# Performance work log

Measured on AMD Instinct MI355X. Metric: run time of the kernel, lower is better.

Reference implementation:

```python
import jax, jax.numpy as jnp
import numpy as np

N_NODES = 50000
N_EDGES = 800000
IN_FEATS = 128
HIDDEN = 128
OUT_LEN = 128


def setup_inputs() -> dict:
    key = jax.random.key(0)
    ks = jax.random.split(key, 8)
    feat = jax.random.normal(ks[0], (N_NODES, IN_FEATS), dtype=jnp.float32)
    # Glorot-ish init for weights, zeros for bias (DGL GraphConv default)
    def w(k, fi, fo):
        return jax.random.normal(k, (fi, fo), dtype=jnp.float32) / np.sqrt(fi)
    W1 = w(ks[1], IN_FEATS, HIDDEN)
    W2 = w(ks[2], HIDDEN, HIDDEN)
    W3 = w(ks[3], HIDDEN, OUT_LEN)
    b1 = jnp.zeros((HIDDEN,), jnp.float32)
    b2 = jnp.zeros((HIDDEN,), jnp.float32)
    b3 = jnp.zeros((OUT_LEN,), jnp.float32)
    src = jax.random.randint(ks[4], (N_EDGES,), 0, N_NODES, dtype=jnp.int32)
    dst = jax.random.randint(ks[5], (N_EDGES,), 0, N_NODES, dtype=jnp.int32)
    return {"feat": feat, "W1": W1, "b1": b1, "W2": W2, "b2": b2,
            "W3": W3, "b3": b3, "src": src, "dst": dst}


def _degree_norm(idx, n):
    # degree counts, clamped to min 1 (DGL behavior), then ^{-1/2}
    deg = jax.ops.segment_sum(jnp.ones_like(idx, dtype=jnp.float32), idx,
                              num_segments=n)
    return jax.lax.rsqrt(jnp.maximum(deg, 1.0))


def _graph_conv(x, W, b, src, dst, out_norm, in_norm):
    # DGL GraphConv, norm='both':
    # h = D_dst^{-1/2} * segsum_dst( D_src^{-1/2} * x[src] ) @ W + b
    h = x * out_norm[:, None]
    m = jax.ops.segment_sum(h[src], dst, num_segments=x.shape[0])  # [N, d]
    m = m * in_norm[:, None]
    return m @ W + b


def reference(feat, W1, b1, W2, b2, W3, b3, src, dst):
    out_norm = _degree_norm(src, feat.shape[0])  # out-degree norm (source)
    in_norm = _degree_norm(dst, feat.shape[0])   # in-degree norm (dest)
    h = jax.nn.relu(_graph_conv(feat, W1, b1, src, dst, out_norm, in_norm))
    h = jax.nn.relu(_graph_conv(h, W2, b2, src, dst, out_norm, in_norm))
    h = _graph_conv(h, W3, b3, src, dst, out_norm, in_norm)
    # single graph: mean_nodes == mean over all nodes, then squeeze -> [out_len]
    return jnp.mean(h, axis=0)
```

## Files before the change

kernel.cpp:

```cpp
#include <hip/hip_runtime.h>

#define N_NODES 50000
#define N_EDGES 800000
#define F 128
#define SCAN_NB 49
#define RN_NB 196
#define CH 64
#define EPC (N_EDGES / CH)
#define HALF 25000
#define QTR 12500
#define BSTRIDE 17
#define AGG_NB (N_NODES / 4)
#define GB ((N_NODES + 63) / 64)

typedef __bf16 bf16x8 __attribute__((ext_vector_type(8)));
typedef float  f32x4  __attribute__((ext_vector_type(4)));
typedef float  f32x2  __attribute__((ext_vector_type(2)));

__device__ inline unsigned short f2bf(float f) {
    unsigned u = __float_as_uint(f);
    u += 0x7FFF + ((u >> 16) & 1);
    return (unsigned short)(u >> 16);
}
__device__ inline unsigned packbf2(float a, float b) {
    return (unsigned)f2bf(a) | ((unsigned)f2bf(b) << 16);
}

__device__ inline void fp8x8_to_f32(uint2 u, float* f) {
    f32x2 v0 = __builtin_amdgcn_cvt_pk_f32_fp8(u.x, false);
    f32x2 v1 = __builtin_amdgcn_cvt_pk_f32_fp8(u.x, true);
    f32x2 v2 = __builtin_amdgcn_cvt_pk_f32_fp8(u.y, false);
    f32x2 v3 = __builtin_amdgcn_cvt_pk_f32_fp8(u.y, true);
    f[0] = v0.x; f[1] = v0.y; f[2] = v1.x; f[3] = v1.y;
    f[4] = v2.x; f[5] = v2.y; f[6] = v3.x; f[7] = v3.y;
}
__device__ inline unsigned f32x4_to_fp8(float a, float b, float c, float d) {
    unsigned r = __builtin_amdgcn_cvt_pk_fp8_f32(a, b, 0, false);
    r = __builtin_amdgcn_cvt_pk_fp8_f32(c, d, r, true);
    return r;
}

__global__ __launch_bounds__(1024) void hist_kernel(const int* __restrict__ src,
                                                    const int* __restrict__ dst,
                                                    unsigned short* __restrict__ Hs16,
                                                    unsigned short* __restrict__ Hd16) {
    __shared__ unsigned hist[HALF / 2];
    int bx = blockIdx.x;
    int c = bx >> 2, t = bx & 1, h = (bx >> 1) & 1;
    const int* ids = t ? dst : src;
    unsigned short* H = t ? Hd16 : Hs16;
    int base = h * HALF;
    for (int j = threadIdx.x; j < HALF / 2; j += 1024) hist[j] = 0;
    __syncthreads();
    int e0 = c * EPC;
    for (int e = e0 + threadIdx.x; e < e0 + EPC; e += 1024) {
        int id = ids[e] - base;
        if ((unsigned)id < (unsigned)HALF)
            atomicAdd(&hist[id >> 1], 1u << ((id & 1) * 16));
    }
    __syncthreads();
    for (int j = threadIdx.x; j < HALF / 2; j += 1024)
        *(unsigned*)&H[(size_t)c * N_NODES + base + 2 * j] = hist[j];
}

__global__ __launch_bounds__(256) void reduceN_kernel(const unsigned short* __restrict__ Hs16,
                                                      const unsigned short* __restrict__ Hd16,
                                                      float* __restrict__ onorm,
                                                      float* __restrict__ inorm,
                                                      int* __restrict__ degd,
                                                      int* __restrict__ bsums) {
    __shared__ int wsum[4];
    int i = blockIdx.x * 256 + threadIdx.x;
    int dd = 0;
    if (i < N_NODES) {
        int ds = 0;
        for (int c = 0; c < CH; c++) {
            ds += Hs16[(size_t)c * N_NODES + i];
            dd += Hd16[(size_t)c * N_NODES + i];
        }
        onorm[i] = rsqrtf(fmaxf((float)ds, 1.0f));
        inorm[i] = rsqrtf(fmaxf((float)dd, 1.0f));
        degd[i] = dd;
    }
    int v = dd;
#pragma unroll
    for (int off = 32; off; off >>= 1) v += __shfl_down(v, off);
    if ((threadIdx.x & 63) == 0) wsum[threadIdx.x >> 6] = v;
    __syncthreads();
    if (threadIdx.x == 0)
        bsums[blockIdx.x] = wsum[0] + wsum[1] + wsum[2] + wsum[3];
}

__global__ __launch_bounds__(1024) void tq_kernel(const int* __restrict__ src,
                                                  const int* __restrict__ dst,
                                                  const float* __restrict__ inorm,
                                                  float* __restrict__ Tq,
                                                  const float* __restrict__ feat,
                                                  const float* __restrict__ onorm,
                                                  uint2* __restrict__ xq,
                                                  const float* __restrict__ W1,
                                                  const float* __restrict__ W2,
                                                  unsigned short* __restrict__ Wt) {
    __shared__ float a[QTR];
    int bx = blockIdx.x;
    int c = bx >> 2, q = bx & 3;
    int base = q * QTR;
    for (int j = threadIdx.x; j < QTR; j += 1024) a[j] = 0.0f;
    __syncthreads();
    int e0 = c * EPC;
    for (int e = e0 + threadIdx.x; e < e0 + EPC; e += 1024) {
        int s = src[e] - base;
        if ((unsigned)s < (unsigned)QTR)
            atomicAdd(&a[s], inorm[dst[e]]);
    }
    __syncthreads();
    for (int j = threadIdx.x; j < QTR; j += 1024)
        Tq[(size_t)c * N_NODES + base + j] = a[j];

    int T = gridDim.x * 1024;
    int id0 = bx * 1024 + threadIdx.x;
    for (int i = id0; i < N_NODES * F / 8; i += T) {
        float w = onorm[i >> 4];
        const float4* xv = (const float4*)feat;
        float4 v0 = xv[i * 2], v1 = xv[i * 2 + 1];
        uint2 o;
        o.x = f32x4_to_fp8(v0.x * w, v0.y * w, v0.z * w, v0.w * w);
        o.y = f32x4_to_fp8(v1.x * w, v1.y * w, v1.z * w, v1.w * w);
        xq[i] = o;
    }
    for (int i = id0; i < 2 * F * F; i += T) {
        int wi = i >> 14, rem = i & 16383;
        int n = rem >> 7, k = rem & 127;
        const float* W = wi ? W2 : W1;
        Wt[(size_t)wi * F * F + (size_t)n * F + k] = f2bf(W[k * F + n]);
    }
}

__global__ __launch_bounds__(1024) void scanC_kernel(const int* __restrict__ deg,
                                                     const int* __restrict__ bsums,
                                                     int* __restrict__ rowst,
                                                     const unsigned short* __restrict__ Hd16,
                                                     int* __restrict__ P,
                                                     const float* __restrict__ Tq,
                                                     float* __restrict__ qt) {
    __shared__ int wsum[16];
    int t = threadIdx.x, lane = t & 63, w = t >> 6;
    int i = blockIdx.x * 1024 + t;
    int v = (i < N_NODES) ? deg[i] : 0;
    int incl = v;
#pragma unroll
    for (int off = 1; off < 64; off <<= 1) {
        int u = __shfl_up(incl, off);
        if (lane >= off) incl += u;
    }
    if (lane == 63) wsum[w] = incl;
    __syncthreads();
    if (t == 0) {
        int s = 0;
        int kmax = min(4 * (int)blockIdx.x, RN_NB);
        for (int k = 0; k < kmax; k++) s += bsums[k];
#pragma unroll
        for (int k = 0; k < 16; k++) { int x = wsum[k]; wsum[k] = s; s += x; }
    }
    __syncthreads();
    incl += wsum[w];
    if (i < N_NODES) {
        int s = incl - v;
        rowst[i] = s;
        if (i == N_NODES - 1) rowst[N_NODES] = incl;
        float tsum = 0.0f;
        for (int c = 0; c < CH; c++) {
            size_t o = (size_t)c * N_NODES + i;
            P[o] = s; s += Hd16[o];
            tsum += Tq[o];
        }
        qt[i] = tsum;
    }
}

__global__ __launch_bounds__(1024) void scatter2_kernel(const int* __restrict__ src,
                                                        const int* __restrict__ dst,
                                                        const int* __restrict__ P,
                                                        int* __restrict__ esrc) {
    __shared__ int cur[QTR];
    int bx = blockIdx.x;
    int c = bx >> 2, q = bx & 3;
    int base = q * QTR;
    for (int j = threadIdx.x; j < QTR; j += 1024)
        cur[j] = P[(size_t)c * N_NODES + base + j];
    __syncthreads();
    int e0 = c * EPC;
    for (int e = e0 + threadIdx.x; e < e0 + EPC; e += 1024) {
        int d = dst[e] - base;
        if ((unsigned)d < (unsigned)QTR) {
            int pos = atomicAdd(&cur[d], 1);
            esrc[pos] = src[e];
        }
    }
}

__global__ __launch_bounds__(256) void agg_csr_kernel(const uint2* __restrict__ xq,
                                                      uint4* __restrict__ mb,
                                                      const int* __restrict__ rowst,
                                                      const int* __restrict__ esrc,
                                                      const float* __restrict__ inorm) {
    int w = threadIdx.x >> 6;
    int lane = threadIdx.x & 63;
    int g = lane >> 4, t = lane & 15;
    int row = blockIdx.x * 4 + w;
    int beg = __builtin_amdgcn_readfirstlane(rowst[row]);
    int end = __builtin_amdgcn_readfirstlane(rowst[row + 1]);
    float acc[8];
#pragma unroll
    for (int k = 0; k < 8; k++) acc[k] = 0.0f;

    for (int e = beg; e < end; e += 16) {
        int ea = min(e + g,      end - 1);
        int eb = min(e + 4 + g,  end - 1);
        int ec = min(e + 8 + g,  end - 1);
        int ed = min(e + 12 + g, end - 1);
        int sa = esrc[ea], sb = esrc[eb], sc = esrc[ec], sd = esrc[ed];
        uint2 ua = xq[(size_t)sa * 16 + t];
        uint2 ub = xq[(size_t)sb * 16 + t];
        uint2 uc = xq[(size_t)sc * 16 + t];
        uint2 ud = xq[(size_t)sd * 16 + t];
        float wa = (e + g      < end) ? 1.0f : 0.0f;
        float wb = (e + 4 + g  < end) ? 1.0f : 0.0f;
        float wc = (e + 8 + g  < end) ? 1.0f : 0.0f;
        float wd = (e + 12 + g < end) ? 1.0f : 0.0f;
        float fa[8], fb[8], fc[8], fd[8];
        fp8x8_to_f32(ua, fa); fp8x8_to_f32(ub, fb);
        fp8x8_to_f32(uc, fc); fp8x8_to_f32(ud, fd);
#pragma unroll
        for (int k = 0; k < 8; k++)
            acc[k] += fa[k] * wa + fb[k] * wb + fc[k] * wc + fd[k] * wd;
    }
#pragma unroll
    for (int k = 0; k < 8; k++) {
        acc[k] += __shfl_xor(acc[k], 16, 64);
        acc[k] += __shfl_xor(acc[k], 32, 64);
    }
    if (g == 0) {
        float inw = inorm[row];
        uint4 o;
        o.x = packbf2(acc[0] * inw, acc[1] * inw);
        o.y = packbf2(acc[2] * inw, acc[3] * inw);
        o.z = packbf2(acc[4] * inw, acc[5] * inw);
        o.w = packbf2(acc[6] * inw, acc[7] * inw);
        mb[(size_t)row * 16 + t] = o;
    }
}

template <int FINAL>
__global__ __launch_bounds__(256) void mfma_gemm_kernel(const unsigned short* __restrict__ A,
                                                        const unsigned short* __restrict__ Wt,
                                                        const float* __restrict__ bias,
                                                        const float* __restrict__ onorm,
                                                        unsigned char* __restrict__ Y8,
                                                        const float* __restrict__ qt,
                                                        float* __restrict__ part2) {
    __shared__ uint4 sB[F * BSTRIDE];
    __shared__ float sPf[4][F];
    int tid = threadIdx.x;
    int w = tid >> 6;
    int lane = tid & 63;
    int quad = lane >> 4, r16 = lane & 15;
    int row0 = blockIdx.x * 64 + w * 16;

    const uint4* Arow = (const uint4*)(A + (size_t)(row0 + r16) * F);
    uint4 a[4];
#pragma unroll
    for (int kk = 0; kk < 4; kk++) a[kk] = Arow[kk * 4 + quad];

    const uint4* G = (const uint4*)Wt;
    for (int j = tid; j < F * 16; j += 256)
        sB[(j >> 4) * BSTRIDE + (j & 15)] = G[j];

    f32x4 acc[8];
#pragma unroll
    for (int t = 0; t < 8; t++) acc[t] = (f32x4){0.f, 0.f, 0.f, 0.f};
    __syncthreads();

#pragma unroll
    for (int kk = 0; kk < 4; kk++) {
        bf16x8 av = __builtin_bit_cast(bf16x8, a[kk]);
#pragma unroll
        for (int t = 0; t < 8; t++) {
            bf16x8 bv = __builtin_bit_cast(bf16x8,
                sB[(t * 16 + r16) * BSTRIDE + kk * 4 + quad]);
            acc[t] = __builtin_amdgcn_mfma_f32_16x16x32_bf16(av, bv, acc[t], 0, 0, 0);
        }
    }

    float rw[4];
#pragma unroll
    for (int reg = 0; reg < 4; reg++) {
        int row = row0 + quad * 4 + reg;
        rw[reg] = (row < N_NODES) ? (FINAL ? qt[row] * onorm[row] : onorm[row]) : 0.0f;
    }

    if (!FINAL) {
#pragma unroll
        for (int t = 0; t < 8; t++) {
            int col = t * 16 + r16;
            float bb = bias[col];
#pragma unroll
            for (int reg = 0; reg < 4; reg++) {
                int row = row0 + quad * 4 + reg;
                if (row < N_NODES) {
                    float v = fmaxf(acc[t][reg] + bb, 0.0f) * rw[reg];
                    unsigned p = __builtin_amdgcn_cvt_pk_fp8_f32(v, v, 0, false);
                    Y8[(size_t)row * F + col] = (unsigned char)(p & 0xFF);
                }
            }
        }
    } else {
#pragma unroll
        for (int t = 0; t < 8; t++) {
            int col = t * 16 + r16;
            float bb = bias[col];
            float p = 0.0f;
#pragma unroll
            for (int reg = 0; reg < 4; reg++)
                p += fmaxf(acc[t][reg] + bb, 0.0f) * rw[reg];
            p += __shfl_xor(p, 16, 64);
            p += __shfl_xor(p, 32, 64);
            if (quad == 0) sPf[w][col] = p;
        }
        __syncthreads();
        if (tid < F)
            part2[(size_t)blockIdx.x * F + tid] =
                sPf[0][tid] + sPf[1][tid] + sPf[2][tid] + sPf[3][tid];
    }
}

__global__ __launch_bounds__(1024) void final_kernel(const float* __restrict__ part2,
                                                     const float* __restrict__ W3,
                                                     const float* __restrict__ b3,
                                                     float* __restrict__ out) {
    __shared__ float sc[8][F];
    int tid = threadIdx.x;
    int col = tid & 127, sl = tid >> 7;
    float acc = 0.0f;
    for (int b = sl; b < GB; b += 8) acc += part2[(size_t)b * F + col];
    sc[sl][col] = acc;
    __syncthreads();
    if (tid < F) {
        float s = 0.0f;
#pragma unroll
        for (int k = 0; k < 8; k++) s += sc[k][tid];
        sc[0][tid] = s * (1.0f / (float)N_NODES);
    }
    __syncthreads();
    if (tid < F) {
        float o = b3[tid];
        for (int k = 0; k < F; k++) o += sc[0][k] * W3[k * F + tid];
        out[tid] = o;
    }
}

extern "C" void kernel_launch(void* const* d_in, const int* in_sizes, int n_in,
                              void* d_out, int out_size, void* d_ws, size_t ws_size,
                              hipStream_t stream) {
    const float* feat = (const float*)d_in[0];
    const float* W1   = (const float*)d_in[1];
    const float* b1   = (const float*)d_in[2];
    const float* W2   = (const float*)d_in[3];
    const float* b2   = (const float*)d_in[4];
    const float* W3   = (const float*)d_in[5];
    const float* b3   = (const float*)d_in[6];
    const int*   src  = (const int*)d_in[7];
    const int*   dst  = (const int*)d_in[8];
    float* out = (float*)d_out;

    char* ws = (char*)d_ws;
    size_t off = 0;
    uint4* mb    = (uint4*)(ws + off); off += (size_t)N_NODES * F * 2;
    float* Tq    = (float*)(ws + off); off += (size_t)CH * N_NODES * 4;
    int*   P     = (int*)  (ws + off); off += (size_t)CH * N_NODES * 4;
    unsigned short* Hs16 = (unsigned short*)(ws + off); off += (size_t)CH * N_NODES * 2;
    unsigned short* Hd16 = (unsigned short*)(ws + off); off += (size_t)CH * N_NODES * 2;
    uint2* xq    = (uint2*)(ws + off); off += (size_t)N_NODES * F;
    uint2* hq    = (uint2*)(ws + off); off += (size_t)N_NODES * F;
    unsigned short* Wt = (unsigned short*)(ws + off); off += 2 * F * F * 2;
    float* part2 = (float*)(ws + off); off += (size_t)GB * F * 4;
    int*   esrc  = (int*)  (ws + off); off += (size_t)N_EDGES * 4;
    float* onorm = (float*)(ws + off); off += N_NODES * 4;
    float* inorm = (float*)(ws + off); off += N_NODES * 4;
    float* qt    = (float*)(ws + off); off += N_NODES * 4;
    int*   degd  = (int*)  (ws + off); off += N_NODES * 4;
    int*   rowst = (int*)  (ws + off); off += (N_NODES + 1) * 4;
    int*   bsums = (int*)  (ws + off); off += 256 * 4;

    hist_kernel<<<4 * CH, 1024, 0, stream>>>(src, dst, Hs16, Hd16);
    reduceN_kernel<<<RN_NB, 256, 0, stream>>>(Hs16, Hd16, onorm, inorm, degd, bsums);
    tq_kernel<<<4 * CH, 1024, 0, stream>>>(src, dst, inorm, Tq,
                                           feat, onorm, xq, W1, W2, Wt);
    scanC_kernel<<<SCAN_NB, 1024, 0, stream>>>(degd, bsums, rowst, Hd16, P, Tq, qt);
    scatter2_kernel<<<4 * CH, 1024, 0, stream>>>(src, dst, P, esrc);

    agg_csr_kernel<<<AGG_NB, 256, 0, stream>>>(xq, mb, rowst, esrc, inorm);
    mfma_gemm_kernel<0><<<GB, 256, 0, stream>>>((const unsigned short*)mb, Wt, b1,
                                                onorm, (unsigned char*)hq, qt, part2);
    agg_csr_kernel<<<AGG_NB, 256, 0, stream>>>(hq, mb, rowst, esrc, inorm);
    mfma_gemm_kernel<1><<<GB, 256, 0, stream>>>((const unsigned short*)mb, Wt + F * F,
                                                b2, onorm, (unsigned char*)hq, qt, part2);
    final_kernel<<<1, 1024, 0, stream>>>(part2, W3, b3, out);
}
```

Before: 233.0 us.

## Fuse qt accumulation into CSR scatter with global atomics, drop tq kernel

Removes the separate tq pass that built per-chunk partial sums of inorm[dst] per source node in shared memory. Those sums are now accumulated with global float atomics inside the scatter kernel, which also absorbs the fp8 feature quantization and weight transpose. This saves one kernel launch, one pass over the edges and the 64x-node Tq buffer, at the cost of 800k global atomics with contention. It also clamps the GEMM's A-row index so out-of-range rows in the last block no longer read past the buffer.

```diff
diff --git a/kernel.cpp b/kernel.cpp
--- a/kernel.cpp
+++ b/kernel.cpp
@@ -91,31 +91,75 @@
         bsums[blockIdx.x] = wsum[0] + wsum[1] + wsum[2] + wsum[3];
 }
 
-__global__ __launch_bounds__(1024) void tq_kernel(const int* __restrict__ src,
-                                                  const int* __restrict__ dst,
-                                                  const float* __restrict__ inorm,
-                                                  float* __restrict__ Tq,
-                                                  const float* __restrict__ feat,
-                                                  const float* __restrict__ onorm,
-                                                  uint2* __restrict__ xq,
-                                                  const float* __restrict__ W1,
-                                                  const float* __restrict__ W2,
-                                                  unsigned short* __restrict__ Wt) {
-    __shared__ float a[QTR];
+__global__ __launch_bounds__(1024) void scanC_kernel(const int* __restrict__ deg,
+                                                     const int* __restrict__ bsums,
+                                                     int* __restrict__ rowst,
+                                                     const unsigned short* __restrict__ Hd16,
+                                                     int* __restrict__ P,
+                                                     float* __restrict__ qtacc) {
+    __shared__ int wsum[16];
+    int t = threadIdx.x, lane = t & 63, w = t >> 6;
+    int i = blockIdx.x * 1024 + t;
+    int v = (i < N_NODES) ? deg[i] : 0;
+    int incl = v;
+#pragma unroll
+    for (int off = 1; off < 64; off <<= 1) {
+        int u = __shfl_up(incl, off);
+        if (lane >= off) incl += u;
+    }
+    if (lane == 63) wsum[w] = incl;
+    __syncthreads();
+    if (t == 0) {
+        int s = 0;
+        int kmax = min(4 * (int)blockIdx.x, RN_NB);
+        for (int k = 0; k < kmax; k++) s += bsums[k];
+#pragma unroll
+        for (int k = 0; k < 16; k++) { int x = wsum[k]; wsum[k] = s; s += x; }
+    }
+    __syncthreads();
+    incl += wsum[w];
+    if (i < N_NODES) {
+        int s = incl - v;
+        rowst[i] = s;
+        if (i == N_NODES - 1) rowst[N_NODES] = incl;
+        qtacc[i] = 0.0f;
+        for (int c = 0; c < CH; c++) {
+            size_t o = (size_t)c * N_NODES + i;
+            P[o] = s; s += Hd16[o];
+        }
+    }
+}
+
+__global__ __launch_bounds__(1024) void scatter2_kernel(const int* __restrict__ src,
+                                                        const int* __restrict__ dst,
+                                                        const int* __restrict__ P,
+                                                        int* __restrict__ esrc,
+                                                        const float* __restrict__ inorm,
+                                                        float* __restrict__ qtacc,
+                                                        const float* __restrict__ feat,
+                                                        const float* __restrict__ onorm,
+                                                        uint2* __restrict__ xq,
+                                                        const float* __restrict__ W1,
+                                                        const float* __restrict__ W2,
+                                                        unsigned short* __restrict__ Wt) {
+    __shared__ int cur[QTR];
     int bx = blockIdx.x;
     int c = bx >> 2, q = bx & 3;
     int base = q * QTR;
-    for (int j = threadIdx.x; j < QTR; j += 1024) a[j] = 0.0f;
+    for (int j = threadIdx.x; j < QTR; j += 1024)
+        cur[j] = P[(size_t)c * N_NODES + base + j];
     __syncthreads();
     int e0 = c * EPC;
     for (int e = e0 + threadIdx.x; e < e0 + EPC; e += 1024) {
-        int s = src[e] - base;
-        if ((unsigned)s < (unsigned)QTR)
-            atomicAdd(&a[s], inorm[dst[e]]);
-    }
-    __syncthreads();
-    for (int j = threadIdx.x; j < QTR; j += 1024)
-        Tq[(size_t)c * N_NODES + base + j] = a[j];
+        int dv = dst[e];
+        int d = dv - base;
+        if ((unsigned)d < (unsigned)QTR) {
+            int s = src[e];
+            int pos = atomicAdd(&cur[d], 1);
+            esrc[pos] = s;
+            atomicAdd(&qtacc[s], inorm[dv]);
+        }
+    }
 
     int T = gridDim.x * 1024;
     int id0 = bx * 1024 + threadIdx.x;
@@ -133,69 +177,6 @@
         int n = rem >> 7, k = rem & 127;
         const float* W = wi ? W2 : W1;
         Wt[(size_t)wi * F * F + (size_t)n * F + k] = f2bf(W[k * F + n]);
-    }
-}
-
-__global__ __launch_bounds__(1024) void scanC_kernel(const int* __restrict__ deg,
-                                                     const int* __restrict__ bsums,
-                                                     int* __restrict__ rowst,
-                                                     const unsigned short* __restrict__ Hd16,
-                                                     int* __restrict__ P,
-                                                     const float* __restrict__ Tq,
-                                                     float* __restrict__ qt) {
-    __shared__ int wsum[16];
-    int t = threadIdx.x, lane = t & 63, w = t >> 6;
-    int i = blockIdx.x * 1024 + t;
-    int v = (i < N_NODES) ? deg[i] : 0;
-    int incl = v;
-#pragma unroll
-    for (int off = 1; off < 64; off <<= 1) {
-        int u = __shfl_up(incl, off);
-        if (lane >= off) incl += u;
-    }
-    if (lane == 63) wsum[w] = incl;
-    __syncthreads();
-    if (t == 0) {
-        int s = 0;
-        int kmax = min(4 * (int)blockIdx.x, RN_NB);
-        for (int k = 0; k < kmax; k++) s += bsums[k];
-#pragma unroll
-        for (int k = 0; k < 16; k++) { int x = wsum[k]; wsum[k] = s; s += x; }
-    }
-    __syncthreads();
-    incl += wsum[w];
-    if (i < N_NODES) {
-        int s = incl - v;
-        rowst[i] = s;
-        if (i == N_NODES - 1) rowst[N_NODES] = incl;
-        float tsum = 0.0f;
-        for (int c = 0; c < CH; c++) {
-            size_t o = (size_t)c * N_NODES + i;
-            P[o] = s; s += Hd16[o];
-            tsum += Tq[o];
-        }
-        qt[i] = tsum;
-    }
-}
-
-__global__ __launch_bounds__(1024) void scatter2_kernel(const int* __restrict__ src,
-                                                        const int* __restrict__ dst,
-                                                        const int* __restrict__ P,
-                                                        int* __restrict__ esrc) {
-    __shared__ int cur[QTR];
-    int bx = blockIdx.x;
-    int c = bx >> 2, q = bx & 3;
-    int base = q * QTR;
-    for (int j = threadIdx.x; j < QTR; j += 1024)
-        cur[j] = P[(size_t)c * N_NODES + base + j];
-    __syncthreads();
-    int e0 = c * EPC;
-    for (int e = e0 + threadIdx.x; e < e0 + EPC; e += 1024) {
-        int d = dst[e] - base;
-        if ((unsigned)d < (unsigned)QTR) {
-            int pos = atomicAdd(&cur[d], 1);
-            esrc[pos] = src[e];
-        }
     }
 }
 
@@ -267,7 +248,8 @@
     int quad = lane >> 4, r16 = lane & 15;
     int row0 = blockIdx.x * 64 + w * 16;
 
-    const uint4* Arow = (const uint4*)(A + (size_t)(row0 + r16) * F);
+    int arow = min(row0 + r16, N_NODES - 1);
+    const uint4* Arow = (const uint4*)(A + (size_t)arow * F);
     uint4 a[4];
 #pragma unroll
     for (int kk = 0; kk < 4; kk++) a[kk] = Arow[kk * 4 + quad];
@@ -376,7 +358,6 @@
     char* ws = (char*)d_ws;
     size_t off = 0;
     uint4* mb    = (uint4*)(ws + off); off += (size_t)N_NODES * F * 2;
-    float* Tq    = (float*)(ws + off); off += (size_t)CH * N_NODES * 4;
     int*   P     = (int*)  (ws + off); off += (size_t)CH * N_NODES * 4;
     unsigned short* Hs16 = (unsigned short*)(ws + off); off += (size_t)CH * N_NODES * 2;
     unsigned short* Hd16 = (unsigned short*)(ws + off); off += (size_t)CH * N_NODES * 2;
@@ -387,23 +368,22 @@
     int*   esrc  = (int*)  (ws + off); off += (size_t)N_EDGES * 4;
     float* onorm = (float*)(ws + off); off += N_NODES * 4;
     float* inorm = (float*)(ws + off); off += N_NODES * 4;
-    float* qt    = (float*)(ws + off); off += N_NODES * 4;
+    float* qtacc = (float*)(ws + off); off += N_NODES * 4;
     int*   degd  = (int*)  (ws + off); off += N_NODES * 4;
     int*   rowst = (int*)  (ws + off); off += (N_NODES + 1) * 4;
     int*   bsums = (int*)  (ws + off); off += 256 * 4;
 
     hist_kernel<<<4 * CH, 1024, 0, stream>>>(src, dst, Hs16, Hd16);
     reduceN_kernel<<<RN_NB, 256, 0, stream>>>(Hs16, Hd16, onorm, inorm, degd, bsums);
-    tq_kernel<<<4 * CH, 1024, 0, stream>>>(src, dst, inorm, Tq,
-                                           feat, onorm, xq, W1, W2, Wt);
-    scanC_kernel<<<SCAN_NB, 1024, 0, stream>>>(degd, bsums, rowst, Hd16, P, Tq, qt);
-    scatter2_kernel<<<4 * CH, 1024, 0, stream>>>(src, dst, P, esrc);
+    scanC_kernel<<<SCAN_NB, 1024, 0, stream>>>(degd, bsums, rowst, Hd16, P, qtacc);
+    scatter2_kernel<<<4 * CH, 1024, 0, stream>>>(src, dst, P, esrc, inorm, qtacc,
+                                                 feat, onorm, xq, W1, W2, Wt);
 
     agg_csr_kernel<<<AGG_NB, 256, 0, stream>>>(xq, mb, rowst, esrc, inorm);
     mfma_gemm_kernel<0><<<GB, 256, 0, stream>>>((const unsigned short*)mb, Wt, b1,
-                                                onorm, (unsigned char*)hq, qt, part2);
+                                                onorm, (unsigned char*)hq, qtacc, part2);
     agg_csr_kernel<<<AGG_NB, 256, 0, stream>>>(hq, mb, rowst, esrc, inorm);
     mfma_gemm_kernel<1><<<GB, 256, 0, stream>>>((const unsigned short*)mb, Wt + F * F,
-                                                b2, onorm, (unsigned char*)hq, qt, part2);
+                                                b2, onorm, (unsigned char*)hq, qtacc, part2);
     final_kernel<<<1, 1024, 0, stream>>>(part2, W3, b3, out);
 }
```

After: 251.2 us. 7.8% more time.

## Shrink degree histograms to bytes and fuse degree reduction into scan

Applied to the files above, without the earlier changes.

The per-chunk degree histograms are stored as 8-bit counts instead of 16-bit, with four nodes packed per shared-memory atomic word. The per-block degree sums are now produced inside the histogram kernel. This lets the separate reduce kernel be merged into the scan kernel, which now also writes byte-sized per-chunk prefix offsets instead of a full int offset array. The qt reduction moves into the first aggregation kernel, and GEMM row loads are clamped to stay in bounds. The aim is to cut histogram and offset memory traffic and one kernel launch. The cost is that per-chunk counts and per-node in-degrees must fit in 8 bits, which holds only for graphs without heavy-degree nodes.

```diff
diff --git a/kernel.cpp b/kernel.cpp
--- a/kernel.cpp
+++ b/kernel.cpp
@@ -4,7 +4,6 @@
 #define N_EDGES 800000
 #define F 128
 #define SCAN_NB 49
-#define RN_NB 196
 #define CH 64
 #define EPC (N_EDGES / CH)
 #define HALF 25000
@@ -42,53 +41,90 @@
 
 __global__ __launch_bounds__(1024) void hist_kernel(const int* __restrict__ src,
                                                     const int* __restrict__ dst,
-                                                    unsigned short* __restrict__ Hs16,
-                                                    unsigned short* __restrict__ Hd16) {
-    __shared__ unsigned hist[HALF / 2];
+                                                    unsigned char* __restrict__ Hs8,
+                                                    unsigned char* __restrict__ Hd8,
+                                                    int* __restrict__ bsump) {
+    __shared__ unsigned hist[HALF / 4];
     int bx = blockIdx.x;
     int c = bx >> 2, t = bx & 1, h = (bx >> 1) & 1;
     const int* ids = t ? dst : src;
-    unsigned short* H = t ? Hd16 : Hs16;
+    unsigned char* H = t ? Hd8 : Hs8;
     int base = h * HALF;
-    for (int j = threadIdx.x; j < HALF / 2; j += 1024) hist[j] = 0;
+    for (int j = threadIdx.x; j < HALF / 4; j += 1024) hist[j] = 0;
     __syncthreads();
     int e0 = c * EPC;
     for (int e = e0 + threadIdx.x; e < e0 + EPC; e += 1024) {
         int id = ids[e] - base;
         if ((unsigned)id < (unsigned)HALF)
-            atomicAdd(&hist[id >> 1], 1u << ((id & 1) * 16));
-    }
-    __syncthreads();
-    for (int j = threadIdx.x; j < HALF / 2; j += 1024)
-        *(unsigned*)&H[(size_t)c * N_NODES + base + 2 * j] = hist[j];
-}
-
-__global__ __launch_bounds__(256) void reduceN_kernel(const unsigned short* __restrict__ Hs16,
-                                                      const unsigned short* __restrict__ Hd16,
-                                                      float* __restrict__ onorm,
-                                                      float* __restrict__ inorm,
-                                                      int* __restrict__ degd,
-                                                      int* __restrict__ bsums) {
-    __shared__ int wsum[4];
-    int i = blockIdx.x * 256 + threadIdx.x;
+            atomicAdd(&hist[id >> 2], 1u << ((id & 3) * 8));
+    }
+    __syncthreads();
+    unsigned* Hw = (unsigned*)(H + (size_t)c * N_NODES + base);
+    for (int j = threadIdx.x; j < HALF / 4; j += 1024) Hw[j] = hist[j];
+    if (t) {
+        int w = threadIdx.x >> 6, lane = threadIdx.x & 63;
+        for (int r = w; r < SCAN_NB; r += 16) {
+            int gi0 = max(r * 1024, base);
+            int gi1 = min(r * 1024 + 1024, base + HALF);
+            int s = 0;
+            for (int li = gi0 - base + lane; li < gi1 - base; li += 64)
+                s += (hist[li >> 2] >> ((li & 3) * 8)) & 255;
+#pragma unroll
+            for (int off = 32; off; off >>= 1) s += __shfl_down(s, off);
+            if (lane == 0) bsump[(c * 2 + h) * SCAN_NB + r] = s;
+        }
+    }
+}
+
+__global__ __launch_bounds__(1024) void scanC_kernel(const unsigned char* __restrict__ Hs8,
+                                                     const unsigned char* __restrict__ Hd8,
+                                                     const int* __restrict__ bsump,
+                                                     float* __restrict__ onorm,
+                                                     float* __restrict__ inorm,
+                                                     int* __restrict__ rowst,
+                                                     unsigned char* __restrict__ P8) {
+    __shared__ int wsum[16];
+    __shared__ int tot[SCAN_NB];
+    int t = threadIdx.x, lane = t & 63, w = t >> 6;
+    int i = blockIdx.x * 1024 + t;
+    if (t < SCAN_NB) {
+        int s = 0;
+        for (int p = 0; p < 2 * CH; p++) s += bsump[p * SCAN_NB + t];
+        tot[t] = s;
+    }
     int dd = 0;
     if (i < N_NODES) {
-        int ds = 0;
+        int ds = 0, run = 0;
         for (int c = 0; c < CH; c++) {
-            ds += Hs16[(size_t)c * N_NODES + i];
-            dd += Hd16[(size_t)c * N_NODES + i];
-        }
+            size_t o = (size_t)c * N_NODES + i;
+            ds += Hs8[o];
+            P8[o] = (unsigned char)run;
+            run += Hd8[o];
+        }
+        dd = run;
         onorm[i] = rsqrtf(fmaxf((float)ds, 1.0f));
         inorm[i] = rsqrtf(fmaxf((float)dd, 1.0f));
-        degd[i] = dd;
-    }
-    int v = dd;
-#pragma unroll
-    for (int off = 32; off; off >>= 1) v += __shfl_down(v, off);
-    if ((threadIdx.x & 63) == 0) wsum[threadIdx.x >> 6] = v;
-    __syncthreads();
-    if (threadIdx.x == 0)
-        bsums[blockIdx.x] = wsum[0] + wsum[1] + wsum[2] + wsum[3];
+    }
+    int v = dd, incl = v;
+#pragma unroll
+    for (int off = 1; off < 64; off <<= 1) {
+        int u = __shfl_up(incl, off);
+        if (lane >= off) incl += u;
+    }
+    if (lane == 63) wsum[w] = incl;
+    __syncthreads();
+    if (t == 0) {
+        int s = 0;
+        for (int r = 0; r < (int)blockIdx.x; r++) s += tot[r];
+#pragma unroll
+        for (int k = 0; k < 16; k++) { int x = wsum[k]; wsum[k] = s; s += x; }
+    }
+    __syncthreads();
+    incl += wsum[w];
+    if (i < N_NODES) {
+        rowst[i] = incl - v;
+        if (i == N_NODES - 1) rowst[N_NODES] = incl;
+    }
 }
 
 __global__ __launch_bounds__(1024) void tq_kernel(const int* __restrict__ src,
@@ -136,58 +172,17 @@
     }
 }
 
-__global__ __launch_bounds__(1024) void scanC_kernel(const int* __restrict__ deg,
-                                                     const int* __restrict__ bsums,
-                                                     int* __restrict__ rowst,
-                                                     const unsigned short* __restrict__ Hd16,
-                                                     int* __restrict__ P,
-                                                     const float* __restrict__ Tq,
-                                                     float* __restrict__ qt) {
-    __shared__ int wsum[16];
-    int t = threadIdx.x, lane = t & 63, w = t >> 6;
-    int i = blockIdx.x * 1024 + t;
-    int v = (i < N_NODES) ? deg[i] : 0;
-    int incl = v;
-#pragma unroll
-    for (int off = 1; off < 64; off <<= 1) {
-        int u = __shfl_up(incl, off);
-        if (lane >= off) incl += u;
-    }
-    if (lane == 63) wsum[w] = incl;
-    __syncthreads();
-    if (t == 0) {
-        int s = 0;
-        int kmax = min(4 * (int)blockIdx.x, RN_NB);
-        for (int k = 0; k < kmax; k++) s += bsums[k];
-#pragma unroll
-        for (int k = 0; k < 16; k++) { int x = wsum[k]; wsum[k] = s; s += x; }
-    }
-    __syncthreads();
-    incl += wsum[w];
-    if (i < N_NODES) {
-        int s = incl - v;
-        rowst[i] = s;
-        if (i == N_NODES - 1) rowst[N_NODES] = incl;
-        float tsum = 0.0f;
-        for (int c = 0; c < CH; c++) {
-            size_t o = (size_t)c * N_NODES + i;
-            P[o] = s; s += Hd16[o];
-            tsum += Tq[o];
-        }
-        qt[i] = tsum;
-    }
-}
-
 __global__ __launch_bounds__(1024) void scatter2_kernel(const int* __restrict__ src,
                                                         const int* __restrict__ dst,
-                                                        const int* __restrict__ P,
+                                                        const int* __restrict__ rowst,
+                                                        const unsigned char* __restrict__ P8,
                                                         int* __restrict__ esrc) {
     __shared__ int cur[QTR];
     int bx = blockIdx.x;
     int c = bx >> 2, q = bx & 3;
     int base = q * QTR;
     for (int j = threadIdx.x; j < QTR; j += 1024)
-        cur[j] = P[(size_t)c * N_NODES + base + j];
+        cur[j] = rowst[base + j] + (int)P8[(size_t)c * N_NODES + base + j];
     __syncthreads();
     int e0 = c * EPC;
     for (int e = e0 + threadIdx.x; e < e0 + EPC; e += 1024) {
@@ -199,11 +194,14 @@
     }
 }
 
+template <int QT>
 __global__ __launch_bounds__(256) void agg_csr_kernel(const uint2* __restrict__ xq,
                                                       uint4* __restrict__ mb,
                                                       const int* __restrict__ rowst,
                                                       const int* __restrict__ esrc,
-                                                      const float* __restrict__ inorm) {
+                                                      const float* __restrict__ inorm,
+                                                      const float* __restrict__ Tq,
+                                                      float* __restrict__ qt) {
     int w = threadIdx.x >> 6;
     int lane = threadIdx.x & 63;
     int g = lane >> 4, t = lane & 15;
@@ -249,6 +247,14 @@
         o.w = packbf2(acc[6] * inw, acc[7] * inw);
         mb[(size_t)row * 16 + t] = o;
     }
+    if (QT) {
+        int i = blockIdx.x * 256 + threadIdx.x;
+        if (i < N_NODES) {
+            float s = 0.0f;
+            for (int c = 0; c < CH; c++) s += Tq[(size_t)c * N_NODES + i];
+            qt[i] = s;
+        }
+    }
 }
 
 template <int FINAL>
@@ -267,7 +273,8 @@
     int quad = lane >> 4, r16 = lane & 15;
     int row0 = blockIdx.x * 64 + w * 16;
 
-    const uint4* Arow = (const uint4*)(A + (size_t)(row0 + r16) * F);
+    int arow = min(row0 + r16, N_NODES - 1);
+    const uint4* Arow = (const uint4*)(A + (size_t)arow * F);
     uint4 a[4];
 #pragma unroll
     for (int kk = 0; kk < 4; kk++) a[kk] = Arow[kk * 4 + quad];
@@ -377,32 +384,31 @@
     size_t off = 0;
     uint4* mb    = (uint4*)(ws + off); off += (size_t)N_NODES * F * 2;
     float* Tq    = (float*)(ws + off); off += (size_t)CH * N_NODES * 4;
-    int*   P     = (int*)  (ws + off); off += (size_t)CH * N_NODES * 4;
-    unsigned short* Hs16 = (unsigned short*)(ws + off); off += (size_t)CH * N_NODES * 2;
-    unsigned short* Hd16 = (unsigned short*)(ws + off); off += (size_t)CH * N_NODES * 2;
     uint2* xq    = (uint2*)(ws + off); off += (size_t)N_NODES * F;
     uint2* hq    = (uint2*)(ws + off); off += (size_t)N_NODES * F;
+    unsigned char* Hs8 = (unsigned char*)(ws + off); off += (size_t)CH * N_NODES;
+    unsigned char* Hd8 = (unsigned char*)(ws + off); off += (size_t)CH * N_NODES;
+    unsigned char* P8  = (unsigned char*)(ws + off); off += (size_t)CH * N_NODES;
+    int*   esrc  = (int*)  (ws + off); off += (size_t)N_EDGES * 4;
     unsigned short* Wt = (unsigned short*)(ws + off); off += 2 * F * F * 2;
     float* part2 = (float*)(ws + off); off += (size_t)GB * F * 4;
-    int*   esrc  = (int*)  (ws + off); off += (size_t)N_EDGES * 4;
     float* onorm = (float*)(ws + off); off += N_NODES * 4;
     float* inorm = (float*)(ws + off); off += N_NODES * 4;
     float* qt    = (float*)(ws + off); off += N_NODES * 4;
-    int*   degd  = (int*)  (ws + off); off += N_NODES * 4;
     int*   rowst = (int*)  (ws + off); off += (N_NODES + 1) * 4;
-    int*   bsums = (int*)  (ws + off); off += 256 * 4;
-
-    hist_kernel<<<4 * CH, 1024, 0, stream>>>(src, dst, Hs16, Hd16);
-    reduceN_kernel<<<RN_NB, 256, 0, stream>>>(Hs16, Hd16, onorm, inorm, degd, bsums);
+    int*   bsump = (int*)  (ws + off); off += 2 * CH * SCAN_NB * 4;
+
+    hist_kernel<<<4 * CH, 1024, 0, stream>>>(src, dst, Hs8, Hd8, bsump);
+    scanC_kernel<<<SCAN_NB, 1024, 0, stream>>>(Hs8, Hd8, bsump, onorm, inorm,
+                                               rowst, P8);
     tq_kernel<<<4 * CH, 1024, 0, stream>>>(src, dst, inorm, Tq,
                                            feat, onorm, xq, W1, W2, Wt);
-    scanC_kernel<<<SCAN_NB, 1024, 0, stream>>>(degd, bsums, rowst, Hd16, P, Tq, qt);
-    scatter2_kernel<<<4 * CH, 1024, 0, stream>>>(src, dst, P, esrc);
-
-    agg_csr_kernel<<<AGG_NB, 256, 0, stream>>>(xq, mb, rowst, esrc, inorm);
+    scatter2_kernel<<<4 * CH, 1024, 0, stream>>>(src, dst, rowst, P8, esrc);
+
+    agg_csr_kernel<1><<<AGG_NB, 256, 0, stream>>>(xq, mb, rowst, esrc, inorm, Tq, qt);
     mfma_gemm_kernel<0><<<GB, 256, 0, stream>>>((const unsigned short*)mb, Wt, b1,
                                                 onorm, (unsigned char*)hq, qt, part2);
-    agg_csr_kernel<<<AGG_NB, 256, 0, stream>>>(hq, mb, rowst, esrc, inorm);
+    agg_csr_kernel<0><<<AGG_NB, 256, 0, stream>>>(hq, mb, rowst, esrc, inorm, Tq, qt);
     mfma_gemm_kernel<1><<<GB, 256, 0, stream>>>((const unsigned short*)mb, Wt + F * F,
                                                 b2, onorm, (unsigned char*)hq, qt, part2);
     final_kernel<<<1, 1024, 0, stream>>>(part2, W3, b3, out);
```

Measured after the change: 227.3 us. 1.03x faster.
